# Performance work log

Hardware: AMD Instinct MI355X
Metric: run time of the kernel (lower is better)

## Reference

```python
import jax, jax.numpy as jnp
import numpy as np

N = 10000
E = 320000
IN, HID, OUT = 512, 128, 128
HEADS, GC = 4, 64
NEG_SLOPE = 0.2


def setup_inputs() -> dict:
    key = jax.random.key(0)
    ks = jax.random.split(key, 12)
    inp = {
        'x': jax.random.normal(ks[0], (N, IN), dtype=jnp.float32),
        'edge_index': jax.random.randint(ks[1], (2, E), 0, N, dtype=jnp.int64),
        # encoder params
        'W1': jax.random.normal(ks[2], (IN, HID), dtype=jnp.float32) / np.sqrt(IN),
        'b1': jnp.zeros((HID,), dtype=jnp.float32),
        'W2': jax.random.normal(ks[3], (HID, OUT), dtype=jnp.float32) / np.sqrt(HID),
        'b2': jnp.zeros((OUT,), dtype=jnp.float32),
        # GATConv params: lin weight [OUT, HEADS*GC], att vectors [HEADS, GC], bias [HEADS*GC]
        'Wg': jax.random.normal(ks[4], (OUT, HEADS * GC), dtype=jnp.float32) / np.sqrt(OUT),
        'att_src': jax.random.normal(ks[5], (HEADS, GC), dtype=jnp.float32) * 0.1,
        'att_dst': jax.random.normal(ks[6], (HEADS, GC), dtype=jnp.float32) * 0.1,
        'bias_g': jnp.zeros((HEADS * GC,), dtype=jnp.float32),
    }
    return inp


def _forward(x, W1, b1, W2, b2, Wg, att_src, att_dst, bias_g, edge_index):
    # encoder: Linear -> ReLU -> Linear
    h = jax.nn.relu(x @ W1 + b1) @ W2 + b2  # [N, OUT]
    # GATConv adds self-loops by default
    loops = jnp.arange(N, dtype=edge_index.dtype)
    src = jnp.concatenate([edge_index[0], loops])  # message sources j
    dst = jnp.concatenate([edge_index[1], loops])  # message targets i
    # per-head linear transform
    g = (h @ Wg).reshape(N, HEADS, GC)  # [N, H, C]
    a_src = jnp.sum(g * att_src, axis=-1)  # [N, H]
    a_dst = jnp.sum(g * att_dst, axis=-1)  # [N, H]
    e = a_src[src] + a_dst[dst]            # [E+N, H]
    e = jax.nn.leaky_relu(e, NEG_SLOPE)
    # segment softmax over incoming edges of each destination node
    m = jax.ops.segment_max(e, dst, num_segments=N)  # [N, H]
    ex = jnp.exp(e - m[dst])
    s = jax.ops.segment_sum(ex, dst, num_segments=N)  # [N, H]
    alpha = ex / s[dst]                    # [E+N, H]
    # weighted scatter-aggregate of source features
    out = jax.ops.segment_sum(g[src] * alpha[:, :, None], dst, num_segments=N)  # [N, H, C]
    return out.reshape(N, HEADS * GC) + bias_g


def reference(x, edge_index, W1, b1, W2, b2, Wg, att_src, att_dst, bias_g):
    return _forward(x, W1, b1, W2, b2, Wg, att_src, att_dst, bias_g, edge_index)
```

## Files before the change

### kernel.cpp

```cpp
#include <hip/hip_runtime.h>

#define N_NODES 10000
#define N_EDGES 320000
#define DIM_IN  512
#define DIM_HID 128
#define HC      256
#define NEG_SLOPE 0.2f
#define SLOT    96

typedef short short8 __attribute__((ext_vector_type(8)));
typedef float floatx4 __attribute__((ext_vector_type(4)));

__device__ __forceinline__ unsigned short f2bf(float x) {
  unsigned int u = __float_as_uint(x);
  u += 0x7FFFu + ((u >> 16) & 1u);
  return (unsigned short)(u >> 16);
}

union Sm1 {
  struct { unsigned short As[2][64][40]; unsigned short Bs[2][32][40]; } g;
  struct { float Ast[16][68]; float Bsf[16][64]; } p;
};

__global__ __launch_bounds__(256) void fused1_kernel(
    const float* __restrict__ x, const float* __restrict__ W1,
    const float* __restrict__ b1,
    const float* __restrict__ W2, const float* __restrict__ Wg,
    const float* __restrict__ b2,
    unsigned short* __restrict__ h1b, unsigned short* __restrict__ WfT,
    float* __restrict__ bfuse, int* __restrict__ cursor) {
  __shared__ Sm1 sm;
  const int t = threadIdx.x;
  const int b = blockIdx.x;

  if (b < 628) {
    constexpr int K = DIM_IN, N = DIM_HID, BK = 32;
    const int m0 = (b % 157) * 64, n0 = (b / 157) * 32;
    const int w = t >> 6, L = t & 63, lm = L & 15, q = L >> 4;
    floatx4 acc[2] = {};
    const int ar = t >> 3, ac = (t & 7) * 4;
    const int bcol = (ar & 7) | (((ar >> 3) ^ (t & 3)) << 3);
    float4 va0, va1, vb, va0n, va1n, vbn;
    auto ld = [&](int kb, float4& a0, float4& a1, float4& bw) {
      a0 = (m0 + ar < N_NODES)
          ? *(const float4*)(x + (size_t)(m0 + ar) * K + kb + ac)
          : make_float4(0.f, 0.f, 0.f, 0.f);
      a1 = (m0 + ar + 32 < N_NODES)
          ? *(const float4*)(x + (size_t)(m0 + ar + 32) * K + kb + ac)
          : make_float4(0.f, 0.f, 0.f, 0.f);
      bw = *(const float4*)(W1 + (size_t)(kb + ar) * N + n0 + ac);
    };
    constexpr int NT = K / BK;
    ld(0, va0, va1, vb);
    for (int kt = 0; kt < NT; ++kt) {
      const int p = kt & 1;
      ushort4 s0 = {f2bf(va0.x), f2bf(va0.y), f2bf(va0.z), f2bf(va0.w)};
      ushort4 s1 = {f2bf(va1.x), f2bf(va1.y), f2bf(va1.z), f2bf(va1.w)};
      *(ushort4*)&sm.g.As[p][ar][ac]      = s0;
      *(ushort4*)&sm.g.As[p][ar + 32][ac] = s1;
      sm.g.Bs[p][ac + 0][bcol] = f2bf(vb.x);
      sm.g.Bs[p][ac + 1][bcol] = f2bf(vb.y);
      sm.g.Bs[p][ac + 2][bcol] = f2bf(vb.z);
      sm.g.Bs[p][ac + 3][bcol] = f2bf(vb.w);
      __syncthreads();
      if (kt + 1 < NT) ld((kt + 1) * BK, va0n, va1n, vbn);
      const short8 af = *(const short8*)&sm.g.As[p][w * 16 + lm][q * 8];
#pragma unroll
      for (int nt = 0; nt < 2; ++nt) {
        const int row = nt * 16 + lm;
        const int kg  = q ^ ((row >> 2) & 3);
        const short8 bf = *(const short8*)&sm.g.Bs[p][row][kg * 8];
        acc[nt] = __builtin_amdgcn_mfma_f32_16x16x32_bf16(af, bf, acc[nt], 0, 0, 0);
      }
      va0 = va0n; va1 = va1n; vb = vbn;
    }
    const int row0 = m0 + w * 16 + q * 4;
#pragma unroll
    for (int nt = 0; nt < 2; ++nt) {
      const int col = n0 + nt * 16 + lm;
      const float bv = b1[col];
#pragma unroll
      for (int r = 0; r < 4; ++r)
        if (row0 + r < N_NODES)
          h1b[(size_t)(row0 + r) * N + col] = f2bf(fmaxf(acc[nt][r] + bv, 0.f));
    }
    return;
  }

  const int bp = b - 628;
  {
    const int flat = bp * 256 + t;
    if (flat < (N_NODES + 3) / 4) ((int4*)cursor)[flat] = make_int4(0, 0, 0, 0);
  }
  const int bx = bp >> 2, by = bp & 3;
  const int tx = t & 15, ty = t >> 4;
  const int m0 = bx * 64, n0 = by * 64;
  const int ar = t >> 2, ac4 = (t & 3) * 4;
  const int br = t >> 4, bc4 = (t & 15) * 4;
  const int arow = m0 + ar;
  float acc[4][4] = {};
  float4 av, bv, avn, bvn;
  auto gload = [&](int k0, float4& a4, float4& b4) {
    if (arow < DIM_HID)       a4 = *(const float4*)(W2 + (size_t)arow * DIM_HID + k0 + ac4);
    else if (arow == DIM_HID) a4 = *(const float4*)(b2 + k0 + ac4);
    else                      a4 = make_float4(0.f, 0.f, 0.f, 0.f);
    b4 = *(const float4*)(Wg + (size_t)(k0 + br) * HC + n0 + bc4);
  };
  gload(0, av, bv);
  for (int k0 = 0; k0 < DIM_HID; k0 += 16) {
    sm.p.Ast[ac4 + 0][ar] = av.x; sm.p.Ast[ac4 + 1][ar] = av.y;
    sm.p.Ast[ac4 + 2][ar] = av.z; sm.p.Ast[ac4 + 3][ar] = av.w;
    *(float4*)&sm.p.Bsf[br][bc4] = bv;
    __syncthreads();
    if (k0 + 16 < DIM_HID) gload(k0 + 16, avn, bvn);
#pragma unroll
    for (int kk = 0; kk < 16; ++kk) {
      const float4 a = *(const float4*)&sm.p.Ast[kk][ty * 4];
      const float4 bq = *(const float4*)&sm.p.Bsf[kk][tx * 4];
      const float as[4] = {a.x, a.y, a.z, a.w};
      const float bs[4] = {bq.x, bq.y, bq.z, bq.w};
#pragma unroll
      for (int i = 0; i < 4; ++i)
#pragma unroll
        for (int j = 0; j < 4; ++j) acc[i][j] = fmaf(as[i], bs[j], acc[i][j]);
    }
    __syncthreads();
    av = avn; bv = bvn;
  }
#pragma unroll
  for (int i = 0; i < 4; ++i) {
    const int row = m0 + ty * 4 + i;
#pragma unroll
    for (int j = 0; j < 4; ++j) {
      const int col = n0 + tx * 4 + j;
      if (row < DIM_HID)       WfT[(size_t)col * DIM_HID + row] = f2bf(acc[i][j]);
      else if (row == DIM_HID) bfuse[col] = acc[i][j];
    }
  }
}

__global__ __launch_bounds__(256) void gemm2_kernel(
    const unsigned short* __restrict__ h1b, const unsigned short* __restrict__ WfT,
    const float* __restrict__ bfuse, unsigned short* __restrict__ g,
    const float* __restrict__ att_src, const float* __restrict__ att_dst,
    float* __restrict__ a_src, float* __restrict__ a_dst,
    const int* __restrict__ e_src, const int* __restrict__ e_dst,
    int* __restrict__ cursor, int* __restrict__ src_sorted) {
  constexpr int K = DIM_HID, N = HC, BK = 32;
  __shared__ unsigned short As[2][64][40];
  __shared__ unsigned short Bs[2][64][40];
  const int t = threadIdx.x;
  {
    const int nthr = gridDim.x * gridDim.y * 256;
    const int flat = (blockIdx.y * gridDim.x + blockIdx.x) * 256 + t;
    for (int id = flat; id < N_EDGES + N_NODES; id += nthr) {
      int s, d;
      if (id < N_EDGES) { s = e_src[id]; d = e_dst[id]; }
      else              { s = d = id - N_EDGES; }
      src_sorted[d * SLOT + atomicAdd(&cursor[d], 1)] = s;
    }
  }
  const int m0 = blockIdx.x * 64, n0 = blockIdx.y * 64;
  const int w = t >> 6, L = t & 63, lm = L & 15, q = L >> 4;
  floatx4 acc[4] = {};
  uint4 ab, abn, bb, bbn;
  auto ld = [&](int kb, uint4& va, uint4& vb) {
    va = *(const uint4*)(h1b + (size_t)(m0 + (t >> 2)) * K + kb + (t & 3) * 8);
    vb = *(const uint4*)(WfT + (size_t)(n0 + (t >> 2)) * K + kb + (t & 3) * 8);
  };
  constexpr int NT = K / BK;
  ld(0, ab, bb);
  for (int kt = 0; kt < NT; ++kt) {
    const int p = kt & 1;
    *(uint4*)&As[p][t >> 2][(t & 3) * 8] = ab;
    *(uint4*)&Bs[p][t >> 2][(t & 3) * 8] = bb;
    __syncthreads();
    if (kt + 1 < NT) ld((kt + 1) * BK, abn, bbn);
    const short8 af = *(const short8*)&As[p][w * 16 + lm][q * 8];
#pragma unroll
    for (int nt = 0; nt < 4; ++nt) {
      const short8 bf = *(const short8*)&Bs[p][nt * 16 + lm][q * 8];
      acc[nt] = __builtin_amdgcn_mfma_f32_16x16x32_bf16(af, bf, acc[nt], 0, 0, 0);
    }
    ab = abn; bb = bbn;
  }
  const int row0 = m0 + w * 16 + q * 4;
  const int hh = n0 >> 6;
  float ps[4] = {}, pd[4] = {};
#pragma unroll
  for (int nt = 0; nt < 4; ++nt) {
    const int col = n0 + nt * 16 + lm;
    const float bv = bfuse[col];
    const float as_c = att_src[hh * 64 + nt * 16 + lm];
    const float ad_c = att_dst[hh * 64 + nt * 16 + lm];
#pragma unroll
    for (int r = 0; r < 4; ++r) {
      const float gv = acc[nt][r] + bv;
      if (row0 + r < N_NODES) g[(size_t)(row0 + r) * N + col] = f2bf(gv);
      ps[r] = fmaf(gv, as_c, ps[r]);
      pd[r] = fmaf(gv, ad_c, pd[r]);
    }
  }
#pragma unroll
  for (int r = 0; r < 4; ++r) {
#pragma unroll
    for (int off = 1; off < 16; off <<= 1) {
      ps[r] += __shfl_xor(ps[r], off);
      pd[r] += __shfl_xor(pd[r], off);
    }
    if (lm == 0 && row0 + r < N_NODES) {
      a_src[(row0 + r) * 4 + hh] = ps[r];
      a_dst[(row0 + r) * 4 + hh] = pd[r];
    }
  }
}

__global__ __launch_bounds__(256) void aggregate_kernel(
    const unsigned short* __restrict__ g, const float* __restrict__ a_src,
    const float* __restrict__ a_dst, const int* __restrict__ cursor,
    const int* __restrict__ src_sorted, const float* __restrict__ bias_g,
    float* __restrict__ out) {
  __shared__ int   s_idx[4][SLOT];
  __shared__ float s_w[4][SLOT * 4];
  const int wv   = threadIdx.x >> 6;
  const int lane = threadIdx.x & 63;
  const int node = blockIdx.x * 4 + wv;
  const int start = node * SLOT;
  const int deg   = cursor[node];
  const int degp  = (deg + 3) & ~3;
  const float4 ad = *(const float4*)(a_dst + node * 4);

  for (int j = lane; j < degp; j += 64) {
    int    s  = 0;
    float4 wq = make_float4(0.f, 0.f, 0.f, 0.f);
    if (j < deg) {
      s = src_sorted[start + j];
      const float4 as4 = *(const float4*)(a_src + s * 4);
      float e0 = as4.x + ad.x; e0 = (e0 > 0.f) ? e0 : NEG_SLOPE * e0;
      float e1 = as4.y + ad.y; e1 = (e1 > 0.f) ? e1 : NEG_SLOPE * e1;
      float e2v = as4.z + ad.z; e2v = (e2v > 0.f) ? e2v : NEG_SLOPE * e2v;
      float e3 = as4.w + ad.w; e3 = (e3 > 0.f) ? e3 : NEG_SLOPE * e3;
      wq = make_float4(__expf(e0), __expf(e1), __expf(e2v), __expf(e3));
    }
    s_idx[wv][j] = s;
    *(float4*)&s_w[wv][j * 4] = wq;
  }
  __syncthreads();

  const int e4 = lane >> 4;
  const int c4 = lane & 15;
  const int h  = c4 >> 2;
  const unsigned short* gbase = g + (size_t)c4 * 16;
  float a[16] = {};
  float s_loc = 0.f;
  const int iters = degp >> 2;
#pragma unroll 2
  for (int k = 0; k < iters; ++k) {
    const int j  = 4 * k + e4;
    const int sj = s_idx[wv][j];
    const float w = s_w[wv][j * 4 + h];
    const uint4 g0 = *(const uint4*)(gbase + (size_t)sj * HC);
    const uint4 g1 = *(const uint4*)(gbase + (size_t)sj * HC + 8);
    s_loc += w;
    a[0]  = fmaf(w, __uint_as_float(g0.x << 16),         a[0]);
    a[1]  = fmaf(w, __uint_as_float(g0.x & 0xFFFF0000u), a[1]);
    a[2]  = fmaf(w, __uint_as_float(g0.y << 16),         a[2]);
    a[3]  = fmaf(w, __uint_as_float(g0.y & 0xFFFF0000u), a[3]);
    a[4]  = fmaf(w, __uint_as_float(g0.z << 16),         a[4]);
    a[5]  = fmaf(w, __uint_as_float(g0.z & 0xFFFF0000u), a[5]);
    a[6]  = fmaf(w, __uint_as_float(g0.w << 16),         a[6]);
    a[7]  = fmaf(w, __uint_as_float(g0.w & 0xFFFF0000u), a[7]);
    a[8]  = fmaf(w, __uint_as_float(g1.x << 16),         a[8]);
    a[9]  = fmaf(w, __uint_as_float(g1.x & 0xFFFF0000u), a[9]);
    a[10] = fmaf(w, __uint_as_float(g1.y << 16),         a[10]);
    a[11] = fmaf(w, __uint_as_float(g1.y & 0xFFFF0000u), a[11]);
    a[12] = fmaf(w, __uint_as_float(g1.z << 16),         a[12]);
    a[13] = fmaf(w, __uint_as_float(g1.z & 0xFFFF0000u), a[13]);
    a[14] = fmaf(w, __uint_as_float(g1.w << 16),         a[14]);
    a[15] = fmaf(w, __uint_as_float(g1.w & 0xFFFF0000u), a[15]);
  }
#pragma unroll
  for (int k = 0; k < 16; ++k) {
    a[k] += __shfl_xor(a[k], 16);
    a[k] += __shfl_xor(a[k], 32);
  }
  s_loc += __shfl_xor(s_loc, 16);
  s_loc += __shfl_xor(s_loc, 32);
  if (e4 == 0) {
    const float inv = 1.f / s_loc;
    float* op = out + (size_t)node * HC + c4 * 16;
    const float* bp = bias_g + c4 * 16;
#pragma unroll
    for (int q = 0; q < 4; ++q) {
      const float4 bq = *(const float4*)(bp + q * 4);
      float4 o;
      o.x = a[4 * q + 0] * inv + bq.x;
      o.y = a[4 * q + 1] * inv + bq.y;
      o.z = a[4 * q + 2] * inv + bq.z;
      o.w = a[4 * q + 3] * inv + bq.w;
      *(float4*)(op + q * 4) = o;
    }
  }
}

extern "C" void kernel_launch(void* const* d_in, const int* in_sizes, int n_in,
                              void* d_out, int out_size, void* d_ws, size_t ws_size,
                              hipStream_t stream) {
  const float* x       = (const float*)d_in[0];
  const int*   ei      = (const int*)d_in[1];
  const float* W1      = (const float*)d_in[2];
  const float* b1      = (const float*)d_in[3];
  const float* W2      = (const float*)d_in[4];
  const float* b2      = (const float*)d_in[5];
  const float* Wg      = (const float*)d_in[6];
  const float* att_src = (const float*)d_in[7];
  const float* att_dst = (const float*)d_in[8];
  const float* bias_g  = (const float*)d_in[9];
  float* out = (float*)d_out;

  char* ws = (char*)d_ws;
  unsigned short* h1b = (unsigned short*)ws; ws += (size_t)(N_NODES + 64) * DIM_HID * 2;
  unsigned short* g   = (unsigned short*)ws; ws += (size_t)N_NODES * HC * 2;
  unsigned short* WfT = (unsigned short*)ws; ws += (size_t)HC * DIM_HID * 2;
  float* bfuse   = (float*)ws; ws += (size_t)HC * 4;
  float* a_src   = (float*)ws; ws += (size_t)N_NODES * 4 * 4;
  float* a_dst   = (float*)ws; ws += (size_t)N_NODES * 4 * 4;
  int* cursor    = (int*)ws;   ws += (size_t)N_NODES * 4;
  int* src_sorted= (int*)ws;   ws += (size_t)N_NODES * SLOT * 4;

  const dim3 blk(256);
  fused1_kernel<<<640, blk, 0, stream>>>(
      x, W1, b1, W2, Wg, b2, h1b, WfT, bfuse, cursor);
  gemm2_kernel<<<dim3(157, 4), blk, 0, stream>>>(
      h1b, WfT, bfuse, g, att_src, att_dst, a_src, a_dst,
      ei, ei + N_EDGES, cursor, src_sorted);
  aggregate_kernel<<<(N_NODES + 3) / 4, blk, 0, stream>>>(
      g, a_src, a_dst, cursor, src_sorted, bias_g, out);
}
```

Baseline: 145.0 us.

## Split aggregate kernel channels across two blocks per node group

The aggregation kernel now splits each node's 256 output channels into two halves handled by separate blocks, doubling the grid to 5000 blocks. Each lane loads one 16-byte bf16 chunk instead of two and keeps 8 accumulators instead of 16, which lowers register pressure and raises parallelism for the gather-bound loop. Adjacent blocks are mapped to the same node group's halves so the gathered source rows may be shared in cache. The cost is that the edge-weight prologue (index load, exponentials) is computed twice per node.

New measurement: 145.2 us. About the same (+0.1%).

```diff
diff --git a/kernel.cpp b/kernel.cpp
--- a/kernel.cpp
+++ b/kernel.cpp
@@ -224,7 +224,10 @@
   __shared__ float s_w[4][SLOT * 4];
   const int wv   = threadIdx.x >> 6;
   const int lane = threadIdx.x & 63;
-  const int node = blockIdx.x * 4 + wv;
+  const int q8   = blockIdx.x >> 3;
+  const int r8   = blockIdx.x & 7;
+  const int half = r8 >> 2;
+  const int node = (q8 * 4 + (r8 & 3)) * 4 + wv;
   const int start = node * SLOT;
   const int deg   = cursor[node];
   const int degp  = (deg + 3) & ~3;
@@ -249,38 +252,29 @@
 
   const int e4 = lane >> 4;
   const int c4 = lane & 15;
-  const int h  = c4 >> 2;
-  const unsigned short* gbase = g + (size_t)c4 * 16;
-  float a[16] = {};
+  const int h  = half * 2 + (c4 >> 3);
+  const unsigned short* gbase = g + (size_t)half * 128 + (size_t)c4 * 8;
+  float a[8] = {};
   float s_loc = 0.f;
   const int iters = degp >> 2;
-#pragma unroll 2
+#pragma unroll 4
   for (int k = 0; k < iters; ++k) {
     const int j  = 4 * k + e4;
     const int sj = s_idx[wv][j];
     const float w = s_w[wv][j * 4 + h];
     const uint4 g0 = *(const uint4*)(gbase + (size_t)sj * HC);
-    const uint4 g1 = *(const uint4*)(gbase + (size_t)sj * HC + 8);
     s_loc += w;
-    a[0]  = fmaf(w, __uint_as_float(g0.x << 16),         a[0]);
-    a[1]  = fmaf(w, __uint_as_float(g0.x & 0xFFFF0000u), a[1]);
-    a[2]  = fmaf(w, __uint_as_float(g0.y << 16),         a[2]);
-    a[3]  = fmaf(w, __uint_as_float(g0.y & 0xFFFF0000u), a[3]);
-    a[4]  = fmaf(w, __uint_as_float(g0.z << 16),         a[4]);
-    a[5]  = fmaf(w, __uint_as_float(g0.z & 0xFFFF0000u), a[5]);
-    a[6]  = fmaf(w, __uint_as_float(g0.w << 16),         a[6]);
-    a[7]  = fmaf(w, __uint_as_float(g0.w & 0xFFFF0000u), a[7]);
-    a[8]  = fmaf(w, __uint_as_float(g1.x << 16),         a[8]);
-    a[9]  = fmaf(w, __uint_as_float(g1.x & 0xFFFF0000u), a[9]);
-    a[10] = fmaf(w, __uint_as_float(g1.y << 16),         a[10]);
-    a[11] = fmaf(w, __uint_as_float(g1.y & 0xFFFF0000u), a[11]);
-    a[12] = fmaf(w, __uint_as_float(g1.z << 16),         a[12]);
-    a[13] = fmaf(w, __uint_as_float(g1.z & 0xFFFF0000u), a[13]);
-    a[14] = fmaf(w, __uint_as_float(g1.w << 16),         a[14]);
-    a[15] = fmaf(w, __uint_as_float(g1.w & 0xFFFF0000u), a[15]);
-  }
-#pragma unroll
-  for (int k = 0; k < 16; ++k) {
+    a[0] = fmaf(w, __uint_as_float(g0.x << 16),         a[0]);
+    a[1] = fmaf(w, __uint_as_float(g0.x & 0xFFFF0000u), a[1]);
+    a[2] = fmaf(w, __uint_as_float(g0.y << 16),         a[2]);
+    a[3] = fmaf(w, __uint_as_float(g0.y & 0xFFFF0000u), a[3]);
+    a[4] = fmaf(w, __uint_as_float(g0.z << 16),         a[4]);
+    a[5] = fmaf(w, __uint_as_float(g0.z & 0xFFFF0000u), a[5]);
+    a[6] = fmaf(w, __uint_as_float(g0.w << 16),         a[6]);
+    a[7] = fmaf(w, __uint_as_float(g0.w & 0xFFFF0000u), a[7]);
+  }
+#pragma unroll
+  for (int k = 0; k < 8; ++k) {
     a[k] += __shfl_xor(a[k], 16);
     a[k] += __shfl_xor(a[k], 32);
   }
@@ -288,18 +282,17 @@
   s_loc += __shfl_xor(s_loc, 32);
   if (e4 == 0) {
     const float inv = 1.f / s_loc;
-    float* op = out + (size_t)node * HC + c4 * 16;
-    const float* bp = bias_g + c4 * 16;
-#pragma unroll
-    for (int q = 0; q < 4; ++q) {
-      const float4 bq = *(const float4*)(bp + q * 4);
-      float4 o;
-      o.x = a[4 * q + 0] * inv + bq.x;
-      o.y = a[4 * q + 1] * inv + bq.y;
-      o.z = a[4 * q + 2] * inv + bq.z;
-      o.w = a[4 * q + 3] * inv + bq.w;
-      *(float4*)(op + q * 4) = o;
-    }
+    float* op = out + (size_t)node * HC + half * 128 + c4 * 8;
+    const float* bp = bias_g + half * 128 + c4 * 8;
+    float4 o0, o1;
+    const float4 b0 = *(const float4*)bp;
+    const float4 b1v = *(const float4*)(bp + 4);
+    o0.x = a[0] * inv + b0.x;  o0.y = a[1] * inv + b0.y;
+    o0.z = a[2] * inv + b0.z;  o0.w = a[3] * inv + b0.w;
+    o1.x = a[4] * inv + b1v.x; o1.y = a[5] * inv + b1v.y;
+    o1.z = a[6] * inv + b1v.z; o1.w = a[7] * inv + b1v.w;
+    *(float4*)op = o0;
+    *(float4*)(op + 4) = o1;
   }
 }
 
@@ -334,6 +327,6 @@
   gemm2_kernel<<<dim3(157, 4), blk, 0, stream>>>(
       h1b, WfT, bfuse, g, att_src, att_dst, a_src, a_dst,
       ei, ei + N_EDGES, cursor, src_sorted);
-  aggregate_kernel<<<(N_NODES + 3) / 4, blk, 0, stream>>>(
+  aggregate_kernel<<<5000, blk, 0, stream>>>(
       g, a_src, a_dst, cursor, src_sorted, bias_g, out);
 }
```
